# Kernel tuning notes

Hardware: AMD Instinct MI355X
Metric: run time of the kernel (lower is better)

## Reference

```python
import jax, jax.numpy as jnp
import numpy as np

T, D, E, I, TOP_K = 4096, 2048, 8, 4096, 2

def setup_inputs() -> dict:
    key = jax.random.key(0)
    k1, k2, k3, k4, k5 = jax.random.split(key, 5)
    s = 0.02
    return {
        "hidden_states": jax.random.normal(k1, (T, D), jnp.float32),
        "wr": jax.random.normal(k2, (E, D), jnp.float32) * s,
        "w1": jax.random.normal(k3, (E, I, D), jnp.float32) * s,
        "v1": jax.random.normal(k4, (E, I, D), jnp.float32) * s,
        "w2": jax.random.normal(k5, (E, D, I), jnp.float32) * s,
        "index": 0,
    }

def reference(hidden_states, wr, w1, v1, w2, index):
    # index selects the layer; n_layers == 1 here so weights are already that layer's.
    x = hidden_states.reshape(-1, D)  # [T, D]
    # Router logits + softmax top-k with renormalization (fused_moe semantics)
    logits = x @ wr.T                                  # [T, E]
    probs = jax.nn.softmax(logits, axis=-1)
    topw, topi = jax.lax.top_k(probs, TOP_K)           # [T, K]
    topw = topw / jnp.sum(topw, axis=-1, keepdims=True)
    # Dense per-token gate matrix, zero for non-selected experts
    t_idx = jnp.arange(x.shape[0])[:, None]
    gates = jnp.zeros((x.shape[0], E), x.dtype).at[t_idx, topi].set(topw)  # [T, E]
    # SiLU-GLU experts: (silu(x w1^T) * (x v1^T)) w2^T, combined by gates
    out = jnp.zeros_like(x)
    for e in range(E):  # fixed small expert count
        h = jax.nn.silu(x @ w1[e].T) * (x @ v1[e].T)   # [T, I]
        out = out + gates[:, e:e + 1] * (h @ w2[e].T)  # [T, D]
    return out
```

## Files before the change

### kernel.cpp

```cpp
#include <hip/hip_runtime.h>
#include <hip/hip_bf16.h>
#include <cstdint>


#define T_TOK 4096
#define DHID  2048
#define NEXP  8
#define IDIM  4096
#define NSLOT (T_TOK * 2)

#define BM 128
#define BK 64

typedef __bf16 bf16x8 __attribute__((ext_vector_type(8)));
typedef __bf16 bf16x4 __attribute__((ext_vector_type(4)));
typedef float  f32x4  __attribute__((ext_vector_type(4)));

__device__ __forceinline__ void gload_lds16(const void* g, void* l) {
    __builtin_amdgcn_global_load_lds(
        (const __attribute__((address_space(1))) uint32_t*)g,
        (__attribute__((address_space(3))) uint32_t*)l, 16, 0, 0);
}

__device__ __forceinline__ void cvt8(const float* __restrict__ s, __bf16* __restrict__ d,
                                     size_t i) {
    const float4* sp = (const float4*)(s + i * 8);
    float4 a = sp[0], b = sp[1];
    bf16x8 o;
    o[0]=(__bf16)a.x; o[1]=(__bf16)a.y; o[2]=(__bf16)a.z; o[3]=(__bf16)a.w;
    o[4]=(__bf16)b.x; o[5]=(__bf16)b.y; o[6]=(__bf16)b.z; o[7]=(__bf16)b.w;
    *(bf16x8*)(d + i * 8) = o;
}

__global__ __launch_bounds__(256) void router_cvt_kernel(
    const float* __restrict__ x, const float* __restrict__ wr,
    __bf16* __restrict__ xb, int* __restrict__ topi, float* __restrict__ topg,
    int* __restrict__ cnt,
    const float* __restrict__ w1, __bf16* __restrict__ wb1,
    const float* __restrict__ v1, __bf16* __restrict__ wv1, size_t n8)
{
    if (blockIdx.x >= T_TOK / 4) {
        size_t cb = blockIdx.x - T_TOK / 4;
        size_t gid = cb * 256 + threadIdx.x;
        size_t stride = (size_t)(gridDim.x - T_TOK / 4) * 256;
        for (size_t i = gid; i < n8; i += stride) {
            cvt8(w1, wb1, i);
            cvt8(v1, wv1, i);
        }
        return;
    }
    int wave = threadIdx.x >> 6, lane = threadIdx.x & 63;
    int t = blockIdx.x * 4 + wave;
    const float4* xr = (const float4*)(x + (size_t)t * DHID);
    bf16x4* xbo = (bf16x4*)(xb + (size_t)t * DHID);
    float acc[NEXP];
#pragma unroll
    for (int e = 0; e < NEXP; ++e) acc[e] = 0.f;
#pragma unroll
    for (int j = 0; j < DHID / 256; ++j) {
        int d4 = lane + j * 64;
        float4 v = xr[d4];
        bf16x4 bv;
        bv[0] = (__bf16)v.x; bv[1] = (__bf16)v.y;
        bv[2] = (__bf16)v.z; bv[3] = (__bf16)v.w;
        xbo[d4] = bv;
#pragma unroll
        for (int e = 0; e < NEXP; ++e) {
            float4 w = ((const float4*)(wr + e * DHID))[d4];
            acc[e] += v.x * w.x + v.y * w.y + v.z * w.z + v.w * w.w;
        }
    }
#pragma unroll
    for (int e = 0; e < NEXP; ++e) {
#pragma unroll
        for (int s = 32; s > 0; s >>= 1) acc[e] += __shfl_xor(acc[e], s);
    }
    if (lane == 0) {
        int e0 = 0; float l0 = acc[0];
#pragma unroll
        for (int e = 1; e < NEXP; ++e) if (acc[e] > l0) { l0 = acc[e]; e0 = e; }
        int e1 = -1; float l1 = -3.4e38f;
#pragma unroll
        for (int e = 0; e < NEXP; ++e) if (e != e0 && acc[e] > l1) { l1 = acc[e]; e1 = e; }
        float g0 = 1.f / (1.f + __expf(l1 - l0));
        topi[t * 2] = e0; topi[t * 2 + 1] = e1;
        topg[t * 2] = g0; topg[t * 2 + 1] = 1.f - g0;
        atomicAdd(&cnt[e0], 1); atomicAdd(&cnt[e1], 1);
    }
}

__global__ void scan_kernel(const int* __restrict__ cnt, int* __restrict__ basep,
                            int* __restrict__ fill)
{
    if (threadIdx.x == 0 && blockIdx.x == 0) {
        int s = 0;
#pragma unroll
        for (int e = 0; e < NEXP; ++e) { basep[e] = s; s += cnt[e]; fill[e] = 0; }
    }
}

__global__ __launch_bounds__(256) void assign_kernel(
    const int* __restrict__ topi, const float* __restrict__ topg,
    const int* __restrict__ basep, int* __restrict__ fill,
    int* __restrict__ tok_of_slot, float* __restrict__ gate_of_slot,
    int* __restrict__ slot_of)
{
    int t = blockIdx.x * 256 + threadIdx.x;
    if (t >= T_TOK) return;
#pragma unroll
    for (int k = 0; k < 2; ++k) {
        int e = topi[t * 2 + k];
        int slot = basep[e] + atomicAdd(&fill[e], 1);
        tok_of_slot[slot] = t;
        gate_of_slot[slot] = topg[t * 2 + k];
        slot_of[t * 2 + k] = slot;
    }
}

__global__ __launch_bounds__(256) void convert_kernel(
    const float* __restrict__ src, __bf16* __restrict__ dst, size_t n8)
{
    for (size_t i = (size_t)blockIdx.x * 256 + threadIdx.x; i < n8;
         i += (size_t)gridDim.x * 256) cvt8(src, dst, i);
}

template <int PASS, int KDIM>
__global__ __launch_bounds__(256, 2) void moe_gemm(
    const __bf16* __restrict__ Abase,
    const __bf16* __restrict__ Wa, const __bf16* __restrict__ Wb,
    const int* __restrict__ tok_of_slot, const float* __restrict__ gate_of_slot,
    const int* __restrict__ cnt, const int* __restrict__ basep,
    __bf16* __restrict__ Out,
    const float* __restrict__ cvt_src, __bf16* __restrict__ cvt_dst, size_t cvt_n8)
{
    int e = blockIdx.z;
    if (e >= NEXP) {
        size_t gid = ((size_t)blockIdx.y * gridDim.x + blockIdx.x) * 256 + threadIdx.x;
        size_t stride = (size_t)gridDim.x * gridDim.y * 256;
        for (size_t i = gid; i < cvt_n8; i += stride) cvt8(cvt_src, cvt_dst, i);
        return;
    }
    int ne = cnt[e];
    int m0 = blockIdx.y * BM;
    if (m0 >= ne) return;
    int n0 = blockIdx.x * (PASS == 1 ? 128 : 256);
    int sbase = basep[e] + m0;

    __shared__ __bf16 As[BM * BK];
    __shared__ __bf16 B1s[BM * BK];
    __shared__ __bf16 B2s[BM * BK];
    __shared__ int   toks[BM];
    __shared__ float gates[BM];

    int tid = threadIdx.x, lane = tid & 63, wave = tid >> 6;
    char* AsB = (char*)&As[0];
    char* B1B = (char*)&B1s[0];
    char* B2B = (char*)&B2s[0];

    if (PASS == 1) {
        if (tid < BM) toks[tid] = (m0 + tid < ne) ? tok_of_slot[sbase + tid] : 0;
    } else {
        if (tid < BM) gates[tid] = gate_of_slot[(m0 + tid < ne) ? (sbase + tid) : sbase];
    }
    __syncthreads();

    const __bf16* a_src[4];
    int coff[4];
#pragma unroll
    for (int r = 0; r < 4; ++r) {
        int chunk = wave * 4 + r;
        int arow  = chunk * 8 + (lane >> 3);
        int csw   = (lane & 7) ^ (arow & 7);
        size_t rowbase;
        if (PASS == 1) {
            rowbase = (size_t)toks[arow] * KDIM;
        } else {
            int srow = (m0 + arow < ne) ? (sbase + arow) : sbase;
            rowbase = (size_t)srow * KDIM;
        }
        a_src[r] = Abase + rowbase + csw * 8;
        coff[r]  = chunk * 1024;
    }

    const __bf16* b1_src[4];
    const __bf16* b2_src[4];
    {
        const __bf16* Wae;
        const __bf16* Wbe;
        if (PASS == 1) {
            Wae = Wa + (size_t)e * IDIM * DHID;
            Wbe = Wb + (size_t)e * IDIM * DHID;
        } else {
            Wae = Wa + (size_t)e * DHID * IDIM;
            Wbe = Wae + (size_t)128 * KDIM;
        }
#pragma unroll
        for (int r = 0; r < 4; ++r) {
            int chunk = wave * 4 + r;
            int brow  = chunk * 8 + (lane >> 3);
            int csw   = (lane & 7) ^ (brow & 7);
            b1_src[r] = Wae + (size_t)(n0 + brow) * KDIM + csw * 8;
            b2_src[r] = Wbe + (size_t)(n0 + brow) * KDIM + csw * 8;
        }
    }

    int wr0 = (wave >> 1) * 64, wc0 = (wave & 1) * 64;

    f32x4 acc1[4][4], acc2[4][4];
    f32x4 zf = {0.f, 0.f, 0.f, 0.f};
#pragma unroll
    for (int m = 0; m < 4; ++m)
#pragma unroll
        for (int n = 0; n < 4; ++n) { acc1[m][n] = zf; acc2[m][n] = zf; }

    const int NK = KDIM / BK;
    for (int t = 0; t < NK; ++t) {
        int ko = t * BK;
#pragma unroll
        for (int r = 0; r < 4; ++r) gload_lds16(a_src[r] + ko, AsB + coff[r]);
#pragma unroll
        for (int r = 0; r < 4; ++r) gload_lds16(b1_src[r] + ko, B1B + coff[r]);
#pragma unroll
        for (int r = 0; r < 4; ++r) gload_lds16(b2_src[r] + ko, B2B + coff[r]);
        __syncthreads();
#pragma unroll
        for (int ks = 0; ks < 2; ++ks) {
            int kb = ks * 64 + (lane >> 4) * 16;
            bf16x8 af[4], b1f[4], b2f[4];
#pragma unroll
            for (int m = 0; m < 4; ++m) {
                int row = wr0 + m * 16 + (lane & 15);
                af[m] = *(const bf16x8*)(AsB + row * 128 + (kb ^ ((row & 7) << 4)));
            }
#pragma unroll
            for (int n = 0; n < 4; ++n) {
                int row = wc0 + n * 16 + (lane & 15);
                int off = row * 128 + (kb ^ ((row & 7) << 4));
                b1f[n] = *(const bf16x8*)(B1B + off);
                b2f[n] = *(const bf16x8*)(B2B + off);
            }
#pragma unroll
            for (int m = 0; m < 4; ++m)
#pragma unroll
                for (int n = 0; n < 4; ++n) {
                    acc1[m][n] = __builtin_amdgcn_mfma_f32_16x16x32_bf16(af[m], b1f[n], acc1[m][n], 0, 0, 0);
                    acc2[m][n] = __builtin_amdgcn_mfma_f32_16x16x32_bf16(af[m], b2f[n], acc2[m][n], 0, 0, 0);
                }
        }
        __syncthreads();
    }

#pragma unroll
    for (int m = 0; m < 4; ++m) {
        int rbase = wr0 + m * 16 + ((lane >> 4) * 4);
#pragma unroll
        for (int n = 0; n < 4; ++n) {
            int col = wc0 + n * 16 + (lane & 15);
#pragma unroll
            for (int r = 0; r < 4; ++r) {
                int lrow = rbase + r;
                if (m0 + lrow < ne) {
                    if (PASS == 1) {
                        float a = acc1[m][n][r];
                        float b = acc2[m][n][r];
                        float h = (a / (1.f + __expf(-a))) * b;
                        Out[(size_t)(sbase + lrow) * IDIM + n0 + col] = (__bf16)h;
                    } else {
                        float g = gates[lrow];
                        size_t obase = (size_t)(sbase + lrow) * DHID + n0;
                        Out[obase + col]       = (__bf16)(acc1[m][n][r] * g);
                        Out[obase + 128 + col] = (__bf16)(acc2[m][n][r] * g);
                    }
                }
            }
        }
    }
}

__global__ __launch_bounds__(256) void combine_kernel(
    const __bf16* __restrict__ outslot, const int* __restrict__ slot_of,
    float* __restrict__ out)
{
    int idx = blockIdx.x * 256 + threadIdx.x;
    int t = idx >> 8;
    int c = (idx & 255) * 8;
    int s0 = slot_of[t * 2], s1 = slot_of[t * 2 + 1];
    bf16x8 a = *(const bf16x8*)(outslot + (size_t)s0 * DHID + c);
    bf16x8 b = *(const bf16x8*)(outslot + (size_t)s1 * DHID + c);
    float4 o0, o1;
    o0.x = (float)a[0] + (float)b[0];
    o0.y = (float)a[1] + (float)b[1];
    o0.z = (float)a[2] + (float)b[2];
    o0.w = (float)a[3] + (float)b[3];
    o1.x = (float)a[4] + (float)b[4];
    o1.y = (float)a[5] + (float)b[5];
    o1.z = (float)a[6] + (float)b[6];
    o1.w = (float)a[7] + (float)b[7];
    *(float4*)(out + (size_t)t * DHID + c)     = o0;
    *(float4*)(out + (size_t)t * DHID + c + 4) = o1;
}

extern "C" void kernel_launch(void* const* d_in, const int* in_sizes, int n_in,
                              void* d_out, int out_size, void* d_ws, size_t ws_size,
                              hipStream_t stream)
{
    (void)in_sizes; (void)n_in; (void)out_size;
    const float* x  = (const float*)d_in[0];
    const float* wr = (const float*)d_in[1];
    const float* w1 = (const float*)d_in[2];
    const float* v1 = (const float*)d_in[3];
    const float* w2 = (const float*)d_in[4];
    float* out = (float*)d_out;

    char* ws = (char*)d_ws;
    size_t off = 0;
    auto alloc = [&](size_t bytes) -> void* {
        void* p = ws + off;
        off += bytes;
        off = (off + 255) & ~(size_t)255;
        return p;
    };
    __bf16* xb      = (__bf16*)alloc((size_t)T_TOK * DHID * 2);
    __bf16* H       = (__bf16*)alloc((size_t)NSLOT * IDIM * 2);
    __bf16* outslot = (__bf16*)alloc((size_t)NSLOT * DHID * 2);
    int*    topi    = (int*)  alloc((size_t)T_TOK * 2 * 4);
    float*  topg    = (float*)alloc((size_t)T_TOK * 2 * 4);
    int*    tok_of_slot  = (int*)  alloc((size_t)NSLOT * 4);
    float*  gate_of_slot = (float*)alloc((size_t)NSLOT * 4);
    int*    slot_of = (int*)  alloc((size_t)NSLOT * 4);
    int*    cnt     = (int*)  alloc(NEXP * 4);
    int*    basep   = (int*)  alloc(NEXP * 4);
    int*    fill    = (int*)  alloc(NEXP * 4);

    const size_t EW   = (size_t)IDIM * DHID;
    const size_t WALL = (size_t)NEXP * EW;
    __bf16* wb1 = (__bf16*)alloc(WALL * 2);
    __bf16* wv1 = (__bf16*)alloc(WALL * 2);
    bool roomy = (ws_size >= off + WALL * 2 + (16u << 20));
    __bf16* wb2 = roomy ? (__bf16*)alloc(WALL * 2) : wb1;

    hipMemsetAsync(cnt, 0, NEXP * 4, stream);
    router_cvt_kernel<<<T_TOK / 4 + 4096, 256, 0, stream>>>(
        x, wr, xb, topi, topg, cnt, w1, wb1, v1, wv1, WALL / 8);
    scan_kernel<<<1, 64, 0, stream>>>(cnt, basep, fill);
    assign_kernel<<<T_TOK / 256, 256, 0, stream>>>(topi, topg, basep, fill,
                                                   tok_of_slot, gate_of_slot, slot_of);
    if (roomy) {
        moe_gemm<1, DHID><<<dim3(IDIM / 128, NSLOT / BM, NEXP + 1), 256, 0, stream>>>(
            xb, wb1, wv1, tok_of_slot, gate_of_slot, cnt, basep, H, w2, wb2, WALL / 8);
    } else {
        moe_gemm<1, DHID><<<dim3(IDIM / 128, NSLOT / BM, NEXP), 256, 0, stream>>>(
            xb, wb1, wv1, tok_of_slot, gate_of_slot, cnt, basep, H, nullptr, nullptr, 0);
        convert_kernel<<<2048, 256, 0, stream>>>(w2, wb2, WALL / 8);
    }
    moe_gemm<2, IDIM><<<dim3(DHID / 256, NSLOT / BM, NEXP), 256, 0, stream>>>(
        H, wb2, nullptr, tok_of_slot, gate_of_slot, cnt, basep, outslot,
        nullptr, nullptr, 0);
    combine_kernel<<<(T_TOK * DHID / 8) / 256, 256, 0, stream>>>(outslot, slot_of, out);
}
```

Before: 842.0 us.

## Double-buffer MoE GEMM LDS tiles with 256-row blocks and 512 threads

The MoE GEMM now uses a 256-row M tile with 8 waves per block. Global-to-LDS tile loads are double-buffered, so the loads for tile t+2 are issued while tile t is computed, with explicit vmcnt waits and barriers. The w2 fp32-to-bf16 conversion moves out of the first GEMM's extra grid slice into the router kernel. The aim is to hide load latency and raise reuse of each weight tile, at the cost of more LDS (about 128KB per block), which may limit occupancy, and of more padded rows for experts with few tokens.

```diff
diff --git a/kernel.cpp b/kernel.cpp
--- a/kernel.cpp
+++ b/kernel.cpp
@@ -9,7 +9,7 @@
 #define IDIM  4096
 #define NSLOT (T_TOK * 2)
 
-#define BM 128
+#define BM 256
 #define BK 64
 
 typedef __bf16 bf16x8 __attribute__((ext_vector_type(8)));
@@ -37,7 +37,8 @@
     __bf16* __restrict__ xb, int* __restrict__ topi, float* __restrict__ topg,
     int* __restrict__ cnt,
     const float* __restrict__ w1, __bf16* __restrict__ wb1,
-    const float* __restrict__ v1, __bf16* __restrict__ wv1, size_t n8)
+    const float* __restrict__ v1, __bf16* __restrict__ wv1,
+    const float* __restrict__ w2, __bf16* __restrict__ wb2, size_t n8)
 {
     if (blockIdx.x >= T_TOK / 4) {
         size_t cb = blockIdx.x - T_TOK / 4;
@@ -46,6 +47,7 @@
         for (size_t i = gid; i < n8; i += stride) {
             cvt8(w1, wb1, i);
             cvt8(v1, wv1, i);
+            if (w2) cvt8(w2, wb2, i);
         }
         return;
     }
@@ -125,37 +127,30 @@
 }
 
 template <int PASS, int KDIM>
-__global__ __launch_bounds__(256, 2) void moe_gemm(
+__global__ __launch_bounds__(512, 2) void moe_gemm(
     const __bf16* __restrict__ Abase,
     const __bf16* __restrict__ Wa, const __bf16* __restrict__ Wb,
     const int* __restrict__ tok_of_slot, const float* __restrict__ gate_of_slot,
     const int* __restrict__ cnt, const int* __restrict__ basep,
-    __bf16* __restrict__ Out,
-    const float* __restrict__ cvt_src, __bf16* __restrict__ cvt_dst, size_t cvt_n8)
-{
-    int e = blockIdx.z;
-    if (e >= NEXP) {
-        size_t gid = ((size_t)blockIdx.y * gridDim.x + blockIdx.x) * 256 + threadIdx.x;
-        size_t stride = (size_t)gridDim.x * gridDim.y * 256;
-        for (size_t i = gid; i < cvt_n8; i += stride) cvt8(cvt_src, cvt_dst, i);
-        return;
-    }
+    __bf16* __restrict__ Out)
+{
+    int e  = blockIdx.z;
     int ne = cnt[e];
     int m0 = blockIdx.y * BM;
     if (m0 >= ne) return;
     int n0 = blockIdx.x * (PASS == 1 ? 128 : 256);
     int sbase = basep[e] + m0;
 
-    __shared__ __bf16 As[BM * BK];
-    __shared__ __bf16 B1s[BM * BK];
-    __shared__ __bf16 B2s[BM * BK];
+    __shared__ __bf16 As[2][BM * BK];
+    __shared__ __bf16 B1s[2][128 * BK];
+    __shared__ __bf16 B2s[2][128 * BK];
     __shared__ int   toks[BM];
     __shared__ float gates[BM];
 
     int tid = threadIdx.x, lane = tid & 63, wave = tid >> 6;
-    char* AsB = (char*)&As[0];
-    char* B1B = (char*)&B1s[0];
-    char* B2B = (char*)&B2s[0];
+    char* AsB = (char*)&As[0][0];
+    char* B1B = (char*)&B1s[0][0];
+    char* B2B = (char*)&B2s[0][0];
 
     if (PASS == 1) {
         if (tid < BM) toks[tid] = (m0 + tid < ne) ? tok_of_slot[sbase + tid] : 0;
@@ -165,7 +160,7 @@
     __syncthreads();
 
     const __bf16* a_src[4];
-    int coff[4];
+    int a_coff[4];
 #pragma unroll
     for (int r = 0; r < 4; ++r) {
         int chunk = wave * 4 + r;
@@ -178,12 +173,12 @@
             int srow = (m0 + arow < ne) ? (sbase + arow) : sbase;
             rowbase = (size_t)srow * KDIM;
         }
-        a_src[r] = Abase + rowbase + csw * 8;
-        coff[r]  = chunk * 1024;
-    }
-
-    const __bf16* b1_src[4];
-    const __bf16* b2_src[4];
+        a_src[r]  = Abase + rowbase + csw * 8;
+        a_coff[r] = chunk * 1024;
+    }
+    const __bf16* b1_src[2];
+    const __bf16* b2_src[2];
+    int b_coff[2];
     {
         const __bf16* Wae;
         const __bf16* Wbe;
@@ -195,16 +190,18 @@
             Wbe = Wae + (size_t)128 * KDIM;
         }
 #pragma unroll
-        for (int r = 0; r < 4; ++r) {
-            int chunk = wave * 4 + r;
+        for (int r = 0; r < 2; ++r) {
+            int chunk = wave * 2 + r;
             int brow  = chunk * 8 + (lane >> 3);
             int csw   = (lane & 7) ^ (brow & 7);
             b1_src[r] = Wae + (size_t)(n0 + brow) * KDIM + csw * 8;
             b2_src[r] = Wbe + (size_t)(n0 + brow) * KDIM + csw * 8;
-        }
-    }
-
-    int wr0 = (wave >> 1) * 64, wc0 = (wave & 1) * 64;
+            b_coff[r] = chunk * 1024;
+        }
+    }
+
+    int wm = wave >> 1;
+    int wn = wave & 1;
 
     f32x4 acc1[4][4], acc2[4][4];
     f32x4 zf = {0.f, 0.f, 0.f, 0.f};
@@ -214,30 +211,44 @@
         for (int n = 0; n < 4; ++n) { acc1[m][n] = zf; acc2[m][n] = zf; }
 
     const int NK = KDIM / BK;
+
+#define ISSUE_TILE(T, BUF)                                                        \
+    {                                                                             \
+        int ko_ = (T) * BK;                                                       \
+        _Pragma("unroll")                                                         \
+        for (int r = 0; r < 4; ++r)                                               \
+            gload_lds16(a_src[r] + ko_, AsB + (BUF) * 32768 + a_coff[r]);         \
+        _Pragma("unroll")                                                         \
+        for (int r = 0; r < 2; ++r)                                               \
+            gload_lds16(b1_src[r] + ko_, B1B + (BUF) * 16384 + b_coff[r]);        \
+        _Pragma("unroll")                                                         \
+        for (int r = 0; r < 2; ++r)                                               \
+            gload_lds16(b2_src[r] + ko_, B2B + (BUF) * 16384 + b_coff[r]);        \
+    }
+
+    ISSUE_TILE(0, 0)
+    ISSUE_TILE(1, 1)
+    asm volatile("s_waitcnt vmcnt(8)" ::: "memory");
+    __builtin_amdgcn_s_barrier();
+    asm volatile("" ::: "memory");
+
+    int p = 0;
     for (int t = 0; t < NK; ++t) {
-        int ko = t * BK;
-#pragma unroll
-        for (int r = 0; r < 4; ++r) gload_lds16(a_src[r] + ko, AsB + coff[r]);
-#pragma unroll
-        for (int r = 0; r < 4; ++r) gload_lds16(b1_src[r] + ko, B1B + coff[r]);
-#pragma unroll
-        for (int r = 0; r < 4; ++r) gload_lds16(b2_src[r] + ko, B2B + coff[r]);
-        __syncthreads();
 #pragma unroll
         for (int ks = 0; ks < 2; ++ks) {
             int kb = ks * 64 + (lane >> 4) * 16;
             bf16x8 af[4], b1f[4], b2f[4];
 #pragma unroll
             for (int m = 0; m < 4; ++m) {
-                int row = wr0 + m * 16 + (lane & 15);
-                af[m] = *(const bf16x8*)(AsB + row * 128 + (kb ^ ((row & 7) << 4)));
+                int row = wm * 64 + m * 16 + (lane & 15);
+                af[m] = *(const bf16x8*)(AsB + p * 32768 + row * 128 + (kb ^ ((row & 7) << 4)));
             }
 #pragma unroll
             for (int n = 0; n < 4; ++n) {
-                int row = wc0 + n * 16 + (lane & 15);
+                int row = wn * 64 + n * 16 + (lane & 15);
                 int off = row * 128 + (kb ^ ((row & 7) << 4));
-                b1f[n] = *(const bf16x8*)(B1B + off);
-                b2f[n] = *(const bf16x8*)(B2B + off);
+                b1f[n] = *(const bf16x8*)(B1B + p * 16384 + off);
+                b2f[n] = *(const bf16x8*)(B2B + p * 16384 + off);
             }
 #pragma unroll
             for (int m = 0; m < 4; ++m)
@@ -247,15 +258,27 @@
                     acc2[m][n] = __builtin_amdgcn_mfma_f32_16x16x32_bf16(af[m], b2f[n], acc2[m][n], 0, 0, 0);
                 }
         }
-        __syncthreads();
-    }
+        asm volatile("s_waitcnt lgkmcnt(0)" ::: "memory");
+        __builtin_amdgcn_s_barrier();
+        asm volatile("" ::: "memory");
+        if (t + 2 < NK) {
+            ISSUE_TILE(t + 2, p)
+            asm volatile("s_waitcnt vmcnt(8)" ::: "memory");
+        } else if (t + 1 < NK) {
+            asm volatile("s_waitcnt vmcnt(0)" ::: "memory");
+        }
+        __builtin_amdgcn_s_barrier();
+        asm volatile("" ::: "memory");
+        p ^= 1;
+    }
+#undef ISSUE_TILE
 
 #pragma unroll
     for (int m = 0; m < 4; ++m) {
-        int rbase = wr0 + m * 16 + ((lane >> 4) * 4);
+        int rbase = wm * 64 + m * 16 + ((lane >> 4) * 4);
 #pragma unroll
         for (int n = 0; n < 4; ++n) {
-            int col = wc0 + n * 16 + (lane & 15);
+            int col = wn * 64 + n * 16 + (lane & 15);
 #pragma unroll
             for (int r = 0; r < 4; ++r) {
                 int lrow = rbase + r;
@@ -341,20 +364,15 @@
 
     hipMemsetAsync(cnt, 0, NEXP * 4, stream);
     router_cvt_kernel<<<T_TOK / 4 + 4096, 256, 0, stream>>>(
-        x, wr, xb, topi, topg, cnt, w1, wb1, v1, wv1, WALL / 8);
+        x, wr, xb, topi, topg, cnt,
+        w1, wb1, v1, wv1, roomy ? w2 : nullptr, wb2, WALL / 8);
     scan_kernel<<<1, 64, 0, stream>>>(cnt, basep, fill);
     assign_kernel<<<T_TOK / 256, 256, 0, stream>>>(topi, topg, basep, fill,
                                                    tok_of_slot, gate_of_slot, slot_of);
-    if (roomy) {
-        moe_gemm<1, DHID><<<dim3(IDIM / 128, NSLOT / BM, NEXP + 1), 256, 0, stream>>>(
-            xb, wb1, wv1, tok_of_slot, gate_of_slot, cnt, basep, H, w2, wb2, WALL / 8);
-    } else {
-        moe_gemm<1, DHID><<<dim3(IDIM / 128, NSLOT / BM, NEXP), 256, 0, stream>>>(
-            xb, wb1, wv1, tok_of_slot, gate_of_slot, cnt, basep, H, nullptr, nullptr, 0);
-        convert_kernel<<<2048, 256, 0, stream>>>(w2, wb2, WALL / 8);
-    }
-    moe_gemm<2, IDIM><<<dim3(DHID / 256, NSLOT / BM, NEXP), 256, 0, stream>>>(
-        H, wb2, nullptr, tok_of_slot, gate_of_slot, cnt, basep, outslot,
-        nullptr, nullptr, 0);
+    moe_gemm<1, DHID><<<dim3(IDIM / 128, NSLOT / BM, NEXP), 512, 0, stream>>>(
+        xb, wb1, wv1, tok_of_slot, gate_of_slot, cnt, basep, H);
+    if (!roomy) convert_kernel<<<2048, 256, 0, stream>>>(w2, wb2, WALL / 8);
+    moe_gemm<2, IDIM><<<dim3(DHID / 256, NSLOT / BM, NEXP), 512, 0, stream>>>(
+        H, wb2, nullptr, tok_of_slot, gate_of_slot, cnt, basep, outslot);
     combine_kernel<<<(T_TOK * DHID / 8) / 256, 256, 0, stream>>>(outslot, slot_of, out);
 }
```

After: 924.2 us. 9.8% more time.

## Split expert GEMM pass into halves to overlap weight conversion

Applied to the files above, without the earlier changes.

The router kernel now converts only the first four experts' w1/v1 weights to bf16. The first GEMM pass is split into two launches. The first launch handles experts 0-3 while extra z-blocks convert w1/v1 for experts 4-7. The second launch handles experts 4-7 while extra blocks convert w2. This moves weight-conversion bandwidth behind GEMM compute instead of paying it up front, at the cost of an extra launch and some contention between the conversion and GEMM blocks.

```diff
diff --git a/kernel.cpp b/kernel.cpp
--- a/kernel.cpp
+++ b/kernel.cpp
@@ -130,16 +130,21 @@
     const __bf16* __restrict__ Wa, const __bf16* __restrict__ Wb,
     const int* __restrict__ tok_of_slot, const float* __restrict__ gate_of_slot,
     const int* __restrict__ cnt, const int* __restrict__ basep,
-    __bf16* __restrict__ Out,
-    const float* __restrict__ cvt_src, __bf16* __restrict__ cvt_dst, size_t cvt_n8)
-{
-    int e = blockIdx.z;
-    if (e >= NEXP) {
+    __bf16* __restrict__ Out, int e0, int nexp_act,
+    const float* __restrict__ cs1, __bf16* __restrict__ cd1,
+    const float* __restrict__ cs2, __bf16* __restrict__ cd2, size_t cvt_n8)
+{
+    int ez = blockIdx.z;
+    if (ez >= nexp_act) {
         size_t gid = ((size_t)blockIdx.y * gridDim.x + blockIdx.x) * 256 + threadIdx.x;
         size_t stride = (size_t)gridDim.x * gridDim.y * 256;
-        for (size_t i = gid; i < cvt_n8; i += stride) cvt8(cvt_src, cvt_dst, i);
+        for (size_t i = gid; i < cvt_n8; i += stride) {
+            cvt8(cs1, cd1, i);
+            if (cs2) cvt8(cs2, cd2, i);
+        }
         return;
     }
+    int e  = e0 + ez;
     int ne = cnt[e];
     int m0 = blockIdx.y * BM;
     if (m0 >= ne) return;
@@ -340,21 +345,34 @@
     __bf16* wb2 = roomy ? (__bf16*)alloc(WALL * 2) : wb1;
 
     hipMemsetAsync(cnt, 0, NEXP * 4, stream);
-    router_cvt_kernel<<<T_TOK / 4 + 4096, 256, 0, stream>>>(
-        x, wr, xb, topi, topg, cnt, w1, wb1, v1, wv1, WALL / 8);
-    scan_kernel<<<1, 64, 0, stream>>>(cnt, basep, fill);
-    assign_kernel<<<T_TOK / 256, 256, 0, stream>>>(topi, topg, basep, fill,
-                                                   tok_of_slot, gate_of_slot, slot_of);
     if (roomy) {
-        moe_gemm<1, DHID><<<dim3(IDIM / 128, NSLOT / BM, NEXP + 1), 256, 0, stream>>>(
-            xb, wb1, wv1, tok_of_slot, gate_of_slot, cnt, basep, H, w2, wb2, WALL / 8);
+        router_cvt_kernel<<<T_TOK / 4 + 4096, 256, 0, stream>>>(
+            x, wr, xb, topi, topg, cnt, w1, wb1, v1, wv1, (4 * EW) / 8);
+        scan_kernel<<<1, 64, 0, stream>>>(cnt, basep, fill);
+        assign_kernel<<<T_TOK / 256, 256, 0, stream>>>(topi, topg, basep, fill,
+                                                       tok_of_slot, gate_of_slot, slot_of);
+        moe_gemm<1, DHID><<<dim3(IDIM / 128, NSLOT / BM, 5), 256, 0, stream>>>(
+            xb, wb1, wv1, tok_of_slot, gate_of_slot, cnt, basep, H, 0, 4,
+            w1 + 4 * EW, wb1 + 4 * EW, v1 + 4 * EW, wv1 + 4 * EW, (4 * EW) / 8);
+        moe_gemm<1, DHID><<<dim3(IDIM / 128, NSLOT / BM, 5), 256, 0, stream>>>(
+            xb, wb1, wv1, tok_of_slot, gate_of_slot, cnt, basep, H, 4, 4,
+            w2, wb2, nullptr, nullptr, WALL / 8);
+        moe_gemm<2, IDIM><<<dim3(DHID / 256, NSLOT / BM, NEXP), 256, 0, stream>>>(
+            H, wb2, nullptr, tok_of_slot, gate_of_slot, cnt, basep, outslot, 0, NEXP,
+            nullptr, nullptr, nullptr, nullptr, 0);
     } else {
+        router_cvt_kernel<<<T_TOK / 4 + 4096, 256, 0, stream>>>(
+            x, wr, xb, topi, topg, cnt, w1, wb1, v1, wv1, WALL / 8);
+        scan_kernel<<<1, 64, 0, stream>>>(cnt, basep, fill);
+        assign_kernel<<<T_TOK / 256, 256, 0, stream>>>(topi, topg, basep, fill,
+                                                       tok_of_slot, gate_of_slot, slot_of);
         moe_gemm<1, DHID><<<dim3(IDIM / 128, NSLOT / BM, NEXP), 256, 0, stream>>>(
-            xb, wb1, wv1, tok_of_slot, gate_of_slot, cnt, basep, H, nullptr, nullptr, 0);
+            xb, wb1, wv1, tok_of_slot, gate_of_slot, cnt, basep, H, 0, NEXP,
+            nullptr, nullptr, nullptr, nullptr, 0);
         convert_kernel<<<2048, 256, 0, stream>>>(w2, wb2, WALL / 8);
-    }
-    moe_gemm<2, IDIM><<<dim3(DHID / 256, NSLOT / BM, NEXP), 256, 0, stream>>>(
-        H, wb2, nullptr, tok_of_slot, gate_of_slot, cnt, basep, outslot,
-        nullptr, nullptr, 0);
+        moe_gemm<2, IDIM><<<dim3(DHID / 256, NSLOT / BM, NEXP), 256, 0, stream>>>(
+            H, wb2, nullptr, tok_of_slot, gate_of_slot, cnt, basep, outslot, 0, NEXP,
+            nullptr, nullptr, nullptr, nullptr, 0);
+    }
     combine_kernel<<<(T_TOK * DHID / 8) / 256, 256, 0, stream>>>(outslot, slot_of, out);
 }
```

New measurement: 872.6 us. +3.6%, slower.
